# Kernel tuning notes

Hardware: AMD Instinct MI355X
Metric: run time of the kernel (lower is better)

## Reference

```python
import jax, jax.numpy as jnp
import numpy as np

KH = KW = 3
PAD = 1

def _bilinear(img, ys, xs):
    # img: [B,C,H,W]; ys, xs: [B,K2,H,W] float sample coords (zero padding outside)
    B, C, H, W = img.shape
    y0 = jnp.floor(ys)
    x0 = jnp.floor(xs)
    wy = ys - y0  # frac weights
    wx = xs - x0
    b = jnp.arange(B)[:, None, None, None]

    def gather(yi, xi):
        valid = (yi >= 0) & (yi <= H - 1) & (xi >= 0) & (xi <= W - 1)
        yc = jnp.clip(yi, 0, H - 1).astype(jnp.int32)
        xc = jnp.clip(xi, 0, W - 1).astype(jnp.int32)
        v = img[b, :, yc, xc]  # [B,K2,H,W,C]
        return v * valid[..., None].astype(img.dtype)

    v00 = gather(y0, x0)
    v01 = gather(y0, x0 + 1)
    v10 = gather(y0 + 1, x0)
    v11 = gather(y0 + 1, x0 + 1)
    wy = wy[..., None]
    wx = wx[..., None]
    return ((1 - wy) * (1 - wx) * v00 + (1 - wy) * wx * v01
            + wy * (1 - wx) * v10 + wy * wx * v11)


def _deform_conv(x, offset, weight, bias):
    # torchvision deform_conv2d v1, stride=1, pad=1, dilation=1
    B, C, H, W = x.shape
    O = weight.shape[0]
    K2 = KH * KW
    off = offset.reshape(B, K2, 2, H, W)
    dy, dx = off[:, :, 0], off[:, :, 1]
    ki, kj = jnp.meshgrid(jnp.arange(KH), jnp.arange(KW), indexing='ij')
    ki = ki.reshape(K2).astype(x.dtype)
    kj = kj.reshape(K2).astype(x.dtype)
    hh = jnp.arange(H, dtype=x.dtype)
    ww = jnp.arange(W, dtype=x.dtype)
    ys = hh[None, None, :, None] - PAD + ki[None, :, None, None] + dy
    xs = ww[None, None, None, :] - PAD + kj[None, :, None, None] + dx
    sampled = _bilinear(x, ys, xs)  # [B,K2,H,W,C]
    out = jnp.einsum('bkhwc,ock->bohw', sampled, weight.reshape(O, C, K2))
    return out + bias[None, :, None, None]


def setup_inputs() -> dict:
    key = jax.random.key(0)
    ks = jax.random.split(key, 8)
    B, C, O, H, W = 8, 256, 256, 56, 56
    red = C // 16
    x = jax.random.normal(ks[0], (B, C, H, W), dtype=jnp.float32)
    w_off = jax.random.normal(ks[1], (2 * KH * KW, C, KH, KW), dtype=jnp.float32) * 0.005
    b_off = jax.random.normal(ks[2], (2 * KH * KW,), dtype=jnp.float32) * 0.01
    w_conv = jax.random.normal(ks[3], (O, C, KH, KW), dtype=jnp.float32) * (1.0 / np.sqrt(C * KH * KW))
    b_conv = jax.random.normal(ks[4], (O,), dtype=jnp.float32) * 0.01
    fc1 = jax.random.normal(ks[5], (red, C), dtype=jnp.float32) * (1.0 / np.sqrt(C))
    fc2 = jax.random.normal(ks[6], (C, red), dtype=jnp.float32) * (1.0 / np.sqrt(red))
    return {"x": x, "w_off": w_off, "b_off": b_off, "w_conv": w_conv,
            "b_conv": b_conv, "fc1": fc1, "fc2": fc2}


def reference(x, w_off, b_off, w_conv, b_conv, fc1, fc2):
    # SE gate
    y = jnp.mean(x, axis=(2, 3))                       # [B,C]
    h = jax.nn.relu(y @ fc1.T)                          # [B,C/16]
    s = jax.nn.sigmoid(h @ fc2.T)                       # [B,C]
    xs = x * s[:, :, None, None]
    # offset conv (standard conv2d, pad=1)
    offset = jax.lax.conv_general_dilated(
        xs, w_off, window_strides=(1, 1), padding=[(PAD, PAD), (PAD, PAD)],
        dimension_numbers=('NCHW', 'OIHW', 'NCHW')) + b_off[None, :, None, None]
    out = _deform_conv(xs, offset, w_conv, b_conv)
    return jnp.tanh(out)
```

## Files before the change

### kernel.cpp

```cpp
#include <hip/hip_runtime.h>
#include <math.h>

typedef __attribute__((ext_vector_type(8))) short short8;
typedef __attribute__((ext_vector_type(8))) _Float16 h16x8;
typedef __attribute__((ext_vector_type(4))) float f32x4;

#define BB 8
#define CC 256
#define OO 256
#define HH 56
#define WW 56
#define HWH 3136
#define RED 16

__device__ inline unsigned short f2h(float f) {
    _Float16 h = (_Float16)f;
    return __builtin_bit_cast(unsigned short, h);
}
__device__ inline float h2f(unsigned short u) {
    return (float)__builtin_bit_cast(_Float16, u);
}
__device__ inline unsigned pkrtz(float lo, float hi) {
    return __builtin_bit_cast(unsigned, __builtin_amdgcn_cvt_pkrtz(lo, hi));
}
__device__ inline float fast_tanh(float x) {
    float e = __expf(2.0f * x);
    return 1.0f - 2.0f / (e + 1.0f);
}
__device__ inline void gl2lds16(const void* g, void* l) {
    __builtin_amdgcn_global_load_lds((const __attribute__((address_space(1))) unsigned int*)g,
                                     (__attribute__((address_space(3))) unsigned int*)l, 16, 0, 0);
}
__device__ inline unsigned pkmul_lo(unsigned a, unsigned b) {
    unsigned d;
    asm("v_pk_mul_f16 %0, %1, %2 op_sel:[0,0] op_sel_hi:[1,0]" : "=v"(d) : "v"(a), "v"(b));
    return d;
}
__device__ inline unsigned pkfma_hi(unsigned a, unsigned b, unsigned c) {
    unsigned d;
    asm("v_pk_fma_f16 %0, %1, %2, %3 op_sel:[0,1,0] op_sel_hi:[1,1,1]" : "=v"(d) : "v"(a), "v"(b), "v"(c));
    return d;
}
__device__ inline unsigned pkfma_lo(unsigned a, unsigned b, unsigned c) {
    unsigned d;
    asm("v_pk_fma_f16 %0, %1, %2, %3 op_sel:[0,0,0] op_sel_hi:[1,0,1]" : "=v"(d) : "v"(a), "v"(b), "v"(c));
    return d;
}
__device__ inline unsigned pkmul(unsigned a, unsigned b) {
    unsigned d;
    asm("v_pk_mul_f16 %0, %1, %2" : "=v"(d) : "v"(a), "v"(b));
    return d;
}
__device__ inline void blend16(uint4 q0, uint4 q1, uint4 q2, uint4 q3,
                               uint2 cw, uint4 sp, char* dst) {
    unsigned o0 = pkmul_lo(q0.x, cw.x); o0 = pkfma_hi(q1.x, cw.x, o0);
    o0 = pkfma_lo(q2.x, cw.y, o0); o0 = pkfma_hi(q3.x, cw.y, o0); o0 = pkmul(o0, sp.x);
    unsigned o1 = pkmul_lo(q0.y, cw.x); o1 = pkfma_hi(q1.y, cw.x, o1);
    o1 = pkfma_lo(q2.y, cw.y, o1); o1 = pkfma_hi(q3.y, cw.y, o1); o1 = pkmul(o1, sp.y);
    unsigned o2 = pkmul_lo(q0.z, cw.x); o2 = pkfma_hi(q1.z, cw.x, o2);
    o2 = pkfma_lo(q2.z, cw.y, o2); o2 = pkfma_hi(q3.z, cw.y, o2); o2 = pkmul(o2, sp.z);
    unsigned o3 = pkmul_lo(q0.w, cw.x); o3 = pkfma_hi(q1.w, cw.x, o3);
    o3 = pkfma_lo(q2.w, cw.y, o3); o3 = pkfma_hi(q3.w, cw.y, o3); o3 = pkmul(o3, sp.w);
    *(uint4*)dst = make_uint4(o0, o1, o2, o3);
}

__global__ __launch_bounds__(256) void prep_w(const float* __restrict__ w_conv, const float* __restrict__ w_off,
                                              unsigned short* __restrict__ wbf, unsigned short* __restrict__ wbo,
                                              float* __restrict__ y) {
    int blk = blockIdx.x;
    int tid = threadIdx.x;
    if (blk < 288) {
        int idx = blk * 256 + tid;
        int lane = idx & 63;
        int f = (idx >> 6) & 3;
        int og = (idx >> 8) & 7;
        int t = idx >> 11;
        int kk = t >> 2, cc = t & 3;
        int n = f >> 1, kh = f & 1;
        int o = og * 32 + n * 16 + (lane & 15);
        int cb2 = cc * 64 + kh * 32 + ((lane >> 4) << 3);
        short8 r;
        #pragma unroll
        for (int e = 0; e < 8; ++e) r[e] = (short)f2h(w_conv[(size_t)(o * 256 + cb2 + e) * 9 + kk]);
        *(short8*)(wbf + (size_t)idx * 8) = r;
    } else if (blk < 324) {
        int idx = (blk - 288) * 256 + tid;
        int g = idx & 7;
        int o = (idx >> 3) & 31;
        int t = idx >> 8;
        int kk = t >> 2, cc = t & 3;
        int dst = (((o * 128 + g * 16) ^ ((o & 7) << 4)) >> 1);
        short8 r;
        #pragma unroll
        for (int e = 0; e < 8; ++e) {
            int c = cc * 64 + g * 8 + e;
            r[e] = (o < 18) ? (short)f2h(w_off[(size_t)(o * 256 + c) * 9 + kk]) : (short)0;
        }
        *(short8*)(wbo + (size_t)t * 2048 + dst) = r;
    } else {
        #pragma unroll
        for (int i = 0; i < 8; ++i) y[i * 256 + tid] = 0.f;
    }
}

__global__ __launch_bounds__(256) void prep_xt(const float* __restrict__ x, unsigned short* __restrict__ x_t,
                                               float* __restrict__ y) {
    __shared__ float t[64][65];
    int blk = blockIdx.x;
    int ct = blk & 3;
    int hwt = (blk >> 2) % 49;
    int b = blk / (4 * 49);
    int c0 = ct * 64, hw0 = hwt * 64;
    int tid = threadIdx.x;
    const float* xb = x + ((size_t)(b * CC + c0)) * HWH + hw0;
    #pragma unroll
    for (int it = 0; it < 16; ++it) {
        int idx = it * 256 + tid;
        int c = idx >> 6, px = idx & 63;
        t[c][px] = xb[(size_t)c * HWH + px];
    }
    __syncthreads();
    unsigned short* xo = x_t + ((size_t)(b * HWH + hw0)) * CC + c0;
    #pragma unroll
    for (int it = 0; it < 16; ++it) {
        int idx = it * 256 + tid;
        int px = idx >> 6, c = idx & 63;
        xo[(size_t)px * CC + c] = f2h(t[c][px]);
    }
    int c = tid >> 2, seg = tid & 3;
    float sum = 0.f;
    #pragma unroll
    for (int i = 0; i < 16; ++i) sum += t[c][seg * 16 + i];
    sum += __shfl_down(sum, 1);
    sum += __shfl_down(sum, 2);
    if (seg == 0) atomicAdd(&y[b * 256 + c0 + c], sum);
}

__global__ __launch_bounds__(256) void se_fc(const float* __restrict__ y, const float* __restrict__ fc1,
                                             const float* __restrict__ fc2, float* __restrict__ s) {
    __shared__ float hbuf[BB * RED];
    const float inv = 1.0f / HWH;
    int t = threadIdx.x;
    if (t < BB * RED) {
        int b = t / RED, r = t % RED;
        float acc = 0.f;
        for (int c = 0; c < CC; ++c) acc += (y[b * CC + c] * inv) * fc1[r * CC + c];
        hbuf[t] = fmaxf(acc, 0.f);
    }
    __syncthreads();
    for (int i = t; i < BB * CC; i += 256) {
        int b = i / CC, c = i % CC;
        float acc = 0.f;
        #pragma unroll
        for (int r = 0; r < RED; ++r) acc += hbuf[b * RED + r] * fc2[c * RED + r];
        s[i] = 1.0f / (1.0f + expf(-acc));
    }
}

__global__ __launch_bounds__(256) void offset_mfma(const unsigned short* __restrict__ x_t,
                                                   const float* __restrict__ s,
                                                   const unsigned short* __restrict__ wbo,
                                                   const float* __restrict__ b_off,
                                                   int4* __restrict__ ci, uint2* __restrict__ cfh) {
    __shared__ __align__(16) char As[4][4096];
    __shared__ __align__(16) char Bs[4][4096];
    __shared__ float red[128 * 8];
    __shared__ float obuf[18 * 32];
    __shared__ float s_lds[256];
    int blk = blockIdx.x;
    blk = (blk & 7) * 98 + (blk >> 3);
    int b = blk / 98;
    int hw0 = (blk % 98) * 32;
    int tid = threadIdx.x;
    int lane = tid & 63, wv = tid >> 6;
    int ks = wv >> 1, m = wv & 1;
    int r0 = lane & 15, kb = (lane >> 4) << 4;
    int px = tid >> 3, c8 = tid & 7;
    int hwp = hw0 + px;
    int hp = hwp / 56, wp_ = hwp - hp * 56;
    int awoff = (px * 128 + c8 * 16) ^ ((px & 7) << 4);
    f32x4 zero = {0.f, 0.f, 0.f, 0.f};
    f32x4 acc[2] = {zero, zero};

    s_lds[tid] = s[b * 256 + tid];
    __syncthreads();

    auto buildA = [&](int q, int r, int buf) {
        int t = q * 18 + r;
        int kk = t >> 2, cc = t & 3;
        int hh = hp + kk / 3 - 1, ww = wp_ + kk % 3 - 1;
        short8 v = {0, 0, 0, 0, 0, 0, 0, 0};
        if (hh >= 0 && hh < 56 && ww >= 0 && ww < 56)
            v = *(const short8*)(x_t + (((size_t)(b * HWH + hh * 56 + ww)) << 8) + cc * 64 + c8 * 8);
        const float* sp_ = &s_lds[cc * 64 + c8 * 8];
        unsigned p0 = pkrtz(h2f((unsigned short)v[0]) * sp_[0], h2f((unsigned short)v[1]) * sp_[1]);
        unsigned p1 = pkrtz(h2f((unsigned short)v[2]) * sp_[2], h2f((unsigned short)v[3]) * sp_[3]);
        unsigned p2 = pkrtz(h2f((unsigned short)v[4]) * sp_[4], h2f((unsigned short)v[5]) * sp_[5]);
        unsigned p3 = pkrtz(h2f((unsigned short)v[6]) * sp_[6], h2f((unsigned short)v[7]) * sp_[7]);
        *(uint4*)(As[q * 2 + buf] + awoff) = make_uint4(p0, p1, p2, p3);
    };
    auto stageB = [&](int q, int r, int buf) {
        int t = q * 18 + r;
        gl2lds16(wbo + (size_t)t * 2048 + tid * 8, Bs[q * 2 + buf] + (tid >> 6) * 1024);
    };

    stageB(0, 0, 0); stageB(1, 0, 0);
    buildA(0, 0, 0); buildA(1, 0, 0);
    __syncthreads();

    #pragma unroll 2
    for (int r = 0; r < 18; ++r) {
        int cur = r & 1;
        if (r < 17) {
            stageB(0, r + 1, cur ^ 1); stageB(1, r + 1, cur ^ 1);
            buildA(0, r + 1, cur ^ 1); buildA(1, r + 1, cur ^ 1);
        }
        h16x8 a[2];
        #pragma unroll
        for (int kh = 0; kh < 2; ++kh) {
            int row = m * 16 + r0;
            int ao = (row * 128 + kh * 64 + kb) ^ ((row & 7) << 4);
            a[kh] = __builtin_bit_cast(h16x8, *(const short8*)(As[ks * 2 + cur] + ao));
        }
        #pragma unroll
        for (int n = 0; n < 2; ++n)
            #pragma unroll
            for (int kh = 0; kh < 2; ++kh) {
                int brow = n * 16 + r0;
                int bo = (brow * 128 + kh * 64 + kb) ^ ((brow & 7) << 4);
                h16x8 bv = __builtin_bit_cast(h16x8, *(const short8*)(Bs[ks * 2 + cur] + bo));
                acc[n] = __builtin_amdgcn_mfma_f32_16x16x32_f16(a[kh], bv, acc[n], 0, 0, 0);
            }
        __syncthreads();
    }

    if (ks == 1) {
        #pragma unroll
        for (int n = 0; n < 2; ++n)
            *(f32x4*)&red[(m * 64 + lane) * 8 + n * 4] = acc[n];
    }
    __syncthreads();
    if (ks == 0) {
        #pragma unroll
        for (int n = 0; n < 2; ++n) {
            f32x4 o2 = *(const f32x4*)&red[(m * 64 + lane) * 8 + n * 4];
            acc[n] += o2;
            int o = n * 16 + r0;
            if (o < 18) {
                float bia = b_off[o];
                #pragma unroll
                for (int j = 0; j < 4; ++j)
                    obuf[o * 32 + m * 16 + ((lane >> 4) << 2) + j] = acc[n][j] + bia;
            }
        }
    }
    __syncthreads();
    for (int i = tid; i < 288; i += 256) {
        int pxi = i & 31, kk = i >> 5;
        int hw = hw0 + pxi;
        int h = hw / 56, w = hw - h * 56;
        float dy = obuf[(kk * 2) * 32 + pxi];
        float dx = obuf[(kk * 2 + 1) * 32 + pxi];
        float ys = (float)(h - 1 + kk / 3) + dy;
        float xs = (float)(w - 1 + kk % 3) + dx;
        float y0f = floorf(ys), x0f = floorf(xs);
        float wy = ys - y0f, wx = xs - x0f;
        int y0 = (int)y0f, x0 = (int)x0f;
        int bi[4]; float wt[4];
        #pragma unroll
        for (int j = 0; j < 4; ++j) {
            int yj = y0 + (j >> 1), xj = x0 + (j & 1);
            bool val = yj >= 0 && yj < 56 && xj >= 0 && xj < 56;
            int yc = min(max(yj, 0), 55), xc = min(max(xj, 0), 55);
            wt[j] = val ? ((j >> 1) ? wy : 1.f - wy) * ((j & 1) ? wx : 1.f - wx) : 0.f;
            bi[j] = (b * HWH + yc * 56 + xc) << 8;
        }
        int idx = (b * 9 + kk) * HWH + hw;
        ci[idx] = make_int4(bi[0], bi[1], bi[2], bi[3]);
        cfh[idx] = make_uint2(pkrtz(wt[0], wt[1]), pkrtz(wt[2], wt[3]));
    }
}

__global__ __launch_bounds__(512) void deform_mfma(const unsigned short* __restrict__ x_t,
                                                   const float* __restrict__ s,
                                                   const int4* __restrict__ ci,
                                                   const uint2* __restrict__ cfh,
                                                   const unsigned short* __restrict__ wbf,
                                                   const float* __restrict__ b_conv,
                                                   float* __restrict__ out) {
    __shared__ __align__(16) char As[16384];
    int blk = blockIdx.x;
    blk = (blk & 7) * 49 + (blk >> 3);
    int b = blk / 49;
    int hw0 = (blk % 49) * 64;
    int tid = threadIdx.x;
    int lane = tid & 63, og = tid >> 6;
    int px = tid >> 3, cg = tid & 7;
    int r0 = lane & 15, kb = (lane >> 4) << 4;
    int awoff = px * 128 + (cg * 16 ^ ((px & 7) << 4));
    int cidx0 = b * 9 * HWH + hw0 + px;
    const unsigned short* wbB = wbf + og * 2048 + lane * 8;

    uint4 sp4[4];
    #pragma unroll
    for (int cc = 0; cc < 4; ++cc) {
        float4 s0 = *(const float4*)(s + b * 256 + cc * 64 + cg * 8);
        float4 s1 = *(const float4*)(s + b * 256 + cc * 64 + cg * 8 + 4);
        sp4[cc] = make_uint4(pkrtz(s0.x, s0.y), pkrtz(s0.z, s0.w), pkrtz(s1.x, s1.y), pkrtz(s1.z, s1.w));
    }

    f32x4 zero = {0.f, 0.f, 0.f, 0.f};
    f32x4 acc[4][2];
    #pragma unroll
    for (int m = 0; m < 4; ++m)
        #pragma unroll
        for (int n = 0; n < 2; ++n) acc[m][n] = zero;

    int4 cbL = ci[cidx0];
    uint2 cwB = cfh[cidx0];
    int4 cbN = ci[cidx0 + HWH];
    uint2 cwN = cfh[cidx0 + HWH];

    uint4 crn0[4], crn1[4];
    short8 bv[4];
    const unsigned short* wbK = wbB + 16384;

    {
        int c00 = cg * 8;
        crn0[0] = *(const uint4*)(x_t + cbL.x + c00);
        crn0[1] = *(const uint4*)(x_t + cbL.y + c00);
        crn0[2] = *(const uint4*)(x_t + cbL.z + c00);
        crn0[3] = *(const uint4*)(x_t + cbL.w + c00);
        int c01 = 64 + cg * 8;
        crn1[0] = *(const uint4*)(x_t + cbL.x + c01);
        crn1[1] = *(const uint4*)(x_t + cbL.y + c01);
        crn1[2] = *(const uint4*)(x_t + cbL.z + c01);
        crn1[3] = *(const uint4*)(x_t + cbL.w + c01);
        #pragma unroll
        for (int f = 0; f < 4; ++f) bv[f] = *(const short8*)(wbB + f * 512);
        blend16(crn0[0], crn0[1], crn0[2], crn0[3], cwB, sp4[0], As + awoff);
    }
    __syncthreads();

#define PHASE(CCV, CBLEND, CLOAD) { \
    constexpr int CCc = (CCV); \
    h16x8 a_[4][2]; \
    { constexpr int tb_ = (CCc & 1) * 8192; \
      _Pragma("unroll") for (int m_ = 0; m_ < 4; ++m_) \
      _Pragma("unroll") for (int kh_ = 0; kh_ < 2; ++kh_) { \
        int row_ = m_ * 16 + r0; \
        int ao_ = row_ * 128 + ((kh_ * 64 + kb) ^ ((row_ & 7) << 4)); \
        a_[m_][kh_] = __builtin_bit_cast(h16x8, *(const short8*)(As + tb_ + ao_)); } } \
    _Pragma("unroll") for (int n_ = 0; n_ < 2; ++n_) \
      _Pragma("unroll") for (int kh_ = 0; kh_ < 2; ++kh_) \
        _Pragma("unroll") for (int m_ = 0; m_ < 4; ++m_) \
          acc[m_][n_] = __builtin_amdgcn_mfma_f32_16x16x32_f16(a_[m_][kh_], __builtin_bit_cast(h16x8, bv[n_ * 2 + kh_]), acc[m_][n_], 0, 0, 0); \
    if (kk < 8 || CCc < 3) { \
        _Pragma("unroll") for (int f_ = 0; f_ < 4; ++f_) bv[f_] = *(const short8*)(wbK + f_ * 512); } \
    wbK += 16384; \
    if (kk < 8 || CCc < 3) { \
        if (CCc == 3) cwB = cwN; \
        blend16(CBLEND[0], CBLEND[1], CBLEND[2], CBLEND[3], cwB, sp4[(CCc + 1) & 3], \
                As + ((CCc + 1) & 1) * 8192 + awoff); } \
    if (kk < 8 || CCc < 2) { \
        if (CCc == 2) cbL = cbN; \
        constexpr int c0_ = ((CCc + 2) & 3) * 64; \
        CLOAD[0] = *(const uint4*)(x_t + cbL.x + c0_ + cg * 8); \
        CLOAD[1] = *(const uint4*)(x_t + cbL.y + c0_ + cg * 8); \
        CLOAD[2] = *(const uint4*)(x_t + cbL.z + c0_ + cg * 8); \
        CLOAD[3] = *(const uint4*)(x_t + cbL.w + c0_ + cg * 8); } \
    if (CCc == 1 && kk < 8) { \
        int cidx = cidx0 + (kk + 1) * HWH; \
        cbN = ci[cidx]; cwN = cfh[cidx]; } \
    __syncthreads(); }

    #pragma unroll 1
    for (int kk = 0; kk < 9; ++kk) {
        PHASE(0, crn1, crn0);
        PHASE(1, crn0, crn1);
        PHASE(2, crn1, crn0);
        PHASE(3, crn0, crn1);
    }
#undef PHASE

    #pragma unroll
    for (int n = 0; n < 2; ++n) {
        int o = og * 32 + n * 16 + r0;
        float bia = b_conv[o];
        #pragma unroll
        for (int m = 0; m < 4; ++m) {
            int pxo = hw0 + m * 16 + ((lane >> 4) << 2);
            float4 v;
            v.x = fast_tanh(acc[m][n][0] + bia);
            v.y = fast_tanh(acc[m][n][1] + bia);
            v.z = fast_tanh(acc[m][n][2] + bia);
            v.w = fast_tanh(acc[m][n][3] + bia);
            *(float4*)(out + ((size_t)(b * OO + o)) * HWH + pxo) = v;
        }
    }
}

extern "C" void kernel_launch(void* const* d_in, const int* in_sizes, int n_in,
                              void* d_out, int out_size, void* d_ws, size_t ws_size,
                              hipStream_t stream) {
    const float* x      = (const float*)d_in[0];
    const float* w_off  = (const float*)d_in[1];
    const float* b_off  = (const float*)d_in[2];
    const float* w_conv = (const float*)d_in[3];
    const float* b_conv = (const float*)d_in[4];
    const float* fc1    = (const float*)d_in[5];
    const float* fc2    = (const float*)d_in[6];
    float* out = (float*)d_out;
    float* ws  = (float*)d_ws;

    float* y = ws;
    float* s = y + 2048;
    unsigned short* x_t = (unsigned short*)(s + 2048);
    unsigned short* wbo = x_t + 6422528;
    unsigned short* wbf = wbo + 73728;
    int4*  ci  = (int4*)(wbf + 589824);
    uint2* cfh = (uint2*)(ci + 225792);

    prep_w<<<325, 256, 0, stream>>>(w_conv, w_off, wbf, wbo, y);
    prep_xt<<<BB * 49 * 4, 256, 0, stream>>>(x, x_t, y);
    se_fc<<<1, 256, 0, stream>>>(y, fc1, fc2, s);
    offset_mfma<<<BB * 98, 256, 0, stream>>>(x_t, s, wbo, b_off, ci, cfh);
    deform_mfma<<<BB * 49, 512, 0, stream>>>(x_t, s, ci, cfh, wbf, b_conv, out);
}
```

Before: 102.0 us.

## Deepen deform_mfma pipeline to four LDS stages with fewer barriers

```diff
diff --git a/kernel.cpp b/kernel.cpp
--- a/kernel.cpp
+++ b/kernel.cpp
@@ -288,7 +288,7 @@
                                                    const unsigned short* __restrict__ wbf,
                                                    const float* __restrict__ b_conv,
                                                    float* __restrict__ out) {
-    __shared__ __align__(16) char As[16384];
+    __shared__ __align__(16) char As[32768];
     int blk = blockIdx.x;
     blk = (blk & 7) * 49 + (blk >> 3);
     int b = blk / 49;
@@ -319,67 +319,82 @@
     int4 cbL = ci[cidx0];
     uint2 cwB = cfh[cidx0];
     int4 cbN = ci[cidx0 + HWH];
-    uint2 cwN = cfh[cidx0 + HWH];
+    uint2 cwM = cfh[cidx0 + HWH];
+    uint2 cwP = cwM;
 
     uint4 crn0[4], crn1[4];
     short8 bv[4];
     const unsigned short* wbK = wbB + 16384;
 
     {
+        uint4 q[4];
         int c00 = cg * 8;
-        crn0[0] = *(const uint4*)(x_t + cbL.x + c00);
-        crn0[1] = *(const uint4*)(x_t + cbL.y + c00);
-        crn0[2] = *(const uint4*)(x_t + cbL.z + c00);
-        crn0[3] = *(const uint4*)(x_t + cbL.w + c00);
+        q[0] = *(const uint4*)(x_t + cbL.x + c00);
+        q[1] = *(const uint4*)(x_t + cbL.y + c00);
+        q[2] = *(const uint4*)(x_t + cbL.z + c00);
+        q[3] = *(const uint4*)(x_t + cbL.w + c00);
+        int c02 = 128 + cg * 8;
+        crn0[0] = *(const uint4*)(x_t + cbL.x + c02);
+        crn0[1] = *(const uint4*)(x_t + cbL.y + c02);
+        crn0[2] = *(const uint4*)(x_t + cbL.z + c02);
+        crn0[3] = *(const uint4*)(x_t + cbL.w + c02);
+        int c03 = 192 + cg * 8;
+        crn1[0] = *(const uint4*)(x_t + cbL.x + c03);
+        crn1[1] = *(const uint4*)(x_t + cbL.y + c03);
+        crn1[2] = *(const uint4*)(x_t + cbL.z + c03);
+        crn1[3] = *(const uint4*)(x_t + cbL.w + c03);
+        #pragma unroll
+        for (int f = 0; f < 4; ++f) bv[f] = *(const short8*)(wbB + f * 512);
+        blend16(q[0], q[1], q[2], q[3], cwB, sp4[0], As + awoff);
         int c01 = 64 + cg * 8;
-        crn1[0] = *(const uint4*)(x_t + cbL.x + c01);
-        crn1[1] = *(const uint4*)(x_t + cbL.y + c01);
-        crn1[2] = *(const uint4*)(x_t + cbL.z + c01);
-        crn1[3] = *(const uint4*)(x_t + cbL.w + c01);
-        #pragma unroll
-        for (int f = 0; f < 4; ++f) bv[f] = *(const short8*)(wbB + f * 512);
-        blend16(crn0[0], crn0[1], crn0[2], crn0[3], cwB, sp4[0], As + awoff);
-    }
-    __syncthreads();
-
-#define PHASE(CCV, CBLEND, CLOAD) { \
+        q[0] = *(const uint4*)(x_t + cbL.x + c01);
+        q[1] = *(const uint4*)(x_t + cbL.y + c01);
+        q[2] = *(const uint4*)(x_t + cbL.z + c01);
+        q[3] = *(const uint4*)(x_t + cbL.w + c01);
+        blend16(q[0], q[1], q[2], q[3], cwB, sp4[1], As + 8192 + awoff);
+    }
+    __syncthreads();
+
+#define PHASE(CCV, CRN) { \
     constexpr int CCc = (CCV); \
+    if (CCc == 0) cbL = cbN; \
     h16x8 a_[4][2]; \
-    { constexpr int tb_ = (CCc & 1) * 8192; \
+    { constexpr int tb_ = CCc * 8192; \
       _Pragma("unroll") for (int m_ = 0; m_ < 4; ++m_) \
       _Pragma("unroll") for (int kh_ = 0; kh_ < 2; ++kh_) { \
         int row_ = m_ * 16 + r0; \
         int ao_ = row_ * 128 + ((kh_ * 64 + kb) ^ ((row_ & 7) << 4)); \
         a_[m_][kh_] = __builtin_bit_cast(h16x8, *(const short8*)(As + tb_ + ao_)); } } \
+    __builtin_amdgcn_s_setprio(1); \
     _Pragma("unroll") for (int n_ = 0; n_ < 2; ++n_) \
       _Pragma("unroll") for (int kh_ = 0; kh_ < 2; ++kh_) \
         _Pragma("unroll") for (int m_ = 0; m_ < 4; ++m_) \
           acc[m_][n_] = __builtin_amdgcn_mfma_f32_16x16x32_f16(a_[m_][kh_], __builtin_bit_cast(h16x8, bv[n_ * 2 + kh_]), acc[m_][n_], 0, 0, 0); \
+    __builtin_amdgcn_s_setprio(0); \
     if (kk < 8 || CCc < 3) { \
         _Pragma("unroll") for (int f_ = 0; f_ < 4; ++f_) bv[f_] = *(const short8*)(wbK + f_ * 512); } \
     wbK += 16384; \
-    if (kk < 8 || CCc < 3) { \
-        if (CCc == 3) cwB = cwN; \
-        blend16(CBLEND[0], CBLEND[1], CBLEND[2], CBLEND[3], cwB, sp4[(CCc + 1) & 3], \
-                As + ((CCc + 1) & 1) * 8192 + awoff); } \
+    if (CCc == 2) { cwB = cwM; cwM = cwP; } \
     if (kk < 8 || CCc < 2) { \
-        if (CCc == 2) cbL = cbN; \
-        constexpr int c0_ = ((CCc + 2) & 3) * 64; \
-        CLOAD[0] = *(const uint4*)(x_t + cbL.x + c0_ + cg * 8); \
-        CLOAD[1] = *(const uint4*)(x_t + cbL.y + c0_ + cg * 8); \
-        CLOAD[2] = *(const uint4*)(x_t + cbL.z + c0_ + cg * 8); \
-        CLOAD[3] = *(const uint4*)(x_t + cbL.w + c0_ + cg * 8); } \
-    if (CCc == 1 && kk < 8) { \
-        int cidx = cidx0 + (kk + 1) * HWH; \
-        cbN = ci[cidx]; cwN = cfh[cidx]; } \
-    __syncthreads(); }
+        blend16(CRN[0], CRN[1], CRN[2], CRN[3], cwB, sp4[(CCc + 2) & 3], \
+                As + ((CCc + 2) & 3) * 8192 + awoff); } \
+    if (kk < 8) { \
+        constexpr int c0_ = CCc * 64; \
+        CRN[0] = *(const uint4*)(x_t + cbL.x + c0_ + cg * 8); \
+        CRN[1] = *(const uint4*)(x_t + cbL.y + c0_ + cg * 8); \
+        CRN[2] = *(const uint4*)(x_t + cbL.z + c0_ + cg * 8); \
+        CRN[3] = *(const uint4*)(x_t + cbL.w + c0_ + cg * 8); } \
+    if (CCc == 1 && kk <= 6) { \
+        int cidx = cidx0 + (kk + 2) * HWH; \
+        cbN = ci[cidx]; cwP = cfh[cidx]; } \
+    if (CCc & 1) __syncthreads(); }
 
     #pragma unroll 1
     for (int kk = 0; kk < 9; ++kk) {
-        PHASE(0, crn1, crn0);
-        PHASE(1, crn0, crn1);
-        PHASE(2, crn1, crn0);
-        PHASE(3, crn0, crn1);
+        PHASE(0, crn0);
+        PHASE(1, crn1);
+        PHASE(2, crn0);
+        PHASE(3, crn1);
     }
 #undef PHASE
 
```

After: 102.5 us. Within noise of the previous version (+0.5%).
